# Performance work log

Hardware: AMD Instinct MI355X
Metric: run time of the kernel (lower is better)

Reference implementation:

```python
import jax, jax.numpy as jnp
import numpy as np
from jax import lax

STRIDE = 2  # down_sample_stride
MATMUL_NORM = True


def maxpool2d_5d(x, s):
    # x: [B, T, C, H, W]; kernel=s, stride=s, padding=(s-1)//2 == 0 for s=2
    return lax.reduce_window(
        x, -jnp.inf, lax.max,
        window_dimensions=(1, 1, 1, s, s),
        window_strides=(1, 1, 1, s, s),
        padding='VALID')


def setup_inputs() -> dict:
    key = jax.random.key(0)
    k1, k2, k3, k4 = jax.random.split(key, 4)
    B, T, Ck, Cv, H, W = 2, 4, 64, 256, 64, 64
    return {
        'memory_keys': jax.random.normal(k1, (B, T, Ck, H, W), jnp.float32),
        'memory_values': jax.random.normal(k2, (B, T, Cv, H, W), jnp.float32),
        'query_key': jax.random.normal(k3, (B, Ck, H, W), jnp.float32),
        'query_value': jax.random.normal(k4, (B, Cv, H, W), jnp.float32),
    }


def reference(memory_keys, memory_values, query_key, query_value):
    B, T, Ck, oH, oW = memory_keys.shape
    Cv = memory_values.shape[2]
    # down-sample memory bank (max pool, stride 2, no padding)
    mk = maxpool2d_5d(memory_keys, STRIDE)   # [B,T,Ck,h,w]
    mv = maxpool2d_5d(memory_values, STRIDE) # [B,T,Cv,h,w]
    h, w = mk.shape[-2], mk.shape[-1]
    M = T * h * w
    N = oH * oH  # code uses ori_height*ori_height (square assumed)
    # permute(0,2,1,3,4).view(B,Ck,M).permute(0,2,1) -> [B, M, Ck]
    mk = mk.transpose(0, 2, 1, 3, 4).reshape(B, Ck, M).transpose(0, 2, 1)
    qk = query_key.reshape(B, Ck, N)
    attn = jnp.einsum('bmc,bcn->bmn', mk, qk)  # [B, M, N]
    if MATMUL_NORM:
        attn = attn * (Ck ** -0.5)
    attn = jax.nn.softmax(attn, axis=1)  # softmax over memory positions
    mv = mv.transpose(0, 2, 1, 3, 4).reshape(B, Cv, M)
    memory = jnp.einsum('bcm,bmn->bcn', mv, attn).reshape(B, Cv, oH, oW)
    return jnp.concatenate([query_value, memory], axis=1)  # [B, 2*Cv, H, W]
```

## Files before the change

### kernel.cpp

```cpp
#include <hip/hip_runtime.h>
#include <hip/hip_bf16.h>

typedef unsigned short u16;
typedef unsigned int   u32;
typedef __attribute__((ext_vector_type(8))) short  bf16x8;
typedef __attribute__((ext_vector_type(4))) float  floatx4;

#define NB 2
#define NT 4
#define CK 64
#define CV 256
#define HH 64
#define WW 64
#define MM 4096
#define NN 4096
#define SCALE 0.125f
#define SHIFT 4.0f
#define OUT_B 2097152
#define NW 64
#define NIT 32

__device__ __forceinline__ u16 f2b(float f) {
    __hip_bfloat16 h = __float2bfloat16(f);
    union { __hip_bfloat16 h; u16 u; } v; v.h = h; return v.u;
}

#define PRE_K 65536
#define PRE_V 589824
#define PRE_T 1114112

__global__ void prep(const float* __restrict__ mk, const float* __restrict__ mv,
                     const float4* __restrict__ qv,
                     u16* __restrict__ pk2, u16* __restrict__ vt,
                     float* __restrict__ out) {
    int u = blockIdx.x * 256 + threadIdx.x;
    if (u < PRE_K) {
        int m = u & 4095, cb8 = (u >> 12) & 7, b = u >> 15;
        int t = m >> 10, hh = (m >> 5) & 31, ww = m & 31;
        const float* s0 = mk + ((size_t)((b*NT + t)*CK + cb8*8))*(HH*WW)
                             + (2*hh)*WW + 2*ww;
        bf16x8 fr;
        #pragma unroll
        for (int i = 0; i < 8; ++i) {
            const float* s = s0 + (size_t)i*(HH*WW);
            float2 r0 = *(const float2*)s;
            float2 r1 = *(const float2*)(s + WW);
            fr[i] = (short)f2b(fmaxf(fmaxf(r0.x, r0.y), fmaxf(r1.x, r1.y)));
        }
        *(bf16x8*)(pk2 + ((size_t)(b*8 + cb8)*MM + m)*8) = fr;
    } else if (u < PRE_V) {
        int u2 = u - PRE_K;
        int m4 = u2 & 1023, c = (u2 >> 10) & 255, b = u2 >> 18;
        int t = m4 >> 8, hh = (m4 >> 3) & 31, w8 = m4 & 7;
        const float* s0 = mv + ((size_t)((b*NT + t)*CV + c))*(HH*WW)
                             + (2*hh)*WW + 8*w8;
        float4 a0 = *(const float4*)(s0);
        float4 a1 = *(const float4*)(s0 + 4);
        float4 b0 = *(const float4*)(s0 + WW);
        float4 b1 = *(const float4*)(s0 + WW + 4);
        ushort4 r;
        r.x = f2b(fmaxf(fmaxf(a0.x, a0.y), fmaxf(b0.x, b0.y)));
        r.y = f2b(fmaxf(fmaxf(a0.z, a0.w), fmaxf(b0.z, b0.w)));
        r.z = f2b(fmaxf(fmaxf(a1.x, a1.y), fmaxf(b1.x, b1.y)));
        r.w = f2b(fmaxf(fmaxf(a1.z, a1.w), fmaxf(b1.z, b1.w)));
        *(ushort4*)(vt + ((size_t)(b*CV + c)*MM) + m4*4) = r;
    } else {
        int u3 = u - PRE_V;
        int b = u3 >> 18, ru = u3 & 262143;
        ((float4*)out)[(size_t)b*(OUT_B/4) + ru] = qv[u3];
    }
}

__device__ __forceinline__ void qk_phase(bf16x8 k0, bf16x8 k1,
        const bf16x8 (&qf)[2][4], float (&sacc)[4],
        u16* __restrict__ Pd, int lrow, int cbw, int sw)
{
    #pragma unroll
    for (int t = 0; t < 4; ++t) {
        floatx4 s = __builtin_amdgcn_mfma_f32_16x16x32_bf16(
                        k0, qf[0][t], (floatx4){0.f,0.f,0.f,0.f}, 0, 0, 0);
        s = __builtin_amdgcn_mfma_f32_16x16x32_bf16(k1, qf[1][t], s, 0, 0, 0);
        float p0 = __expf(s[0]*SCALE - SHIFT);
        float p1 = __expf(s[1]*SCALE - SHIFT);
        float p2 = __expf(s[2]*SCALE - SHIFT);
        float p3 = __expf(s[3]*SCALE - SHIFT);
        sacc[t] += (p0 + p1) + (p2 + p3);
        u32 d0 = (u32)f2b(p0) | ((u32)f2b(p1) << 16);
        u32 d1 = (u32)f2b(p2) | ((u32)f2b(p3) << 16);
        *(uint2*)&Pd[(t*16 + lrow)*128 + ((cbw ^ sw) << 2)] = make_uint2(d0, d1);
    }
}

__device__ __forceinline__ void pv_phase(const bf16x8 (&vf)[4],
        floatx4 (&oacc)[4], const u16* __restrict__ Ps,
        int lrow, int quad, int sw)
{
    #pragma unroll
    for (int cc = 0; cc < 4; ++cc) {
        bf16x8 pf[4];
        #pragma unroll
        for (int t = 0; t < 4; ++t) {
            int cb = (cc << 3) + (quad << 1);
            pf[t] = *(const bf16x8*)&Ps[(t*16 + lrow)*128 + ((cb ^ sw) << 2)];
        }
        __builtin_amdgcn_s_setprio(1);
        #pragma unroll
        for (int t = 0; t < 4; ++t)
            oacc[t] = __builtin_amdgcn_mfma_f32_16x16x32_bf16(
                          vf[cc], pf[t], oacc[t], 0, 0, 0);
        __builtin_amdgcn_s_setprio(0);
    }
}

__launch_bounds__(512, 2)
__global__ void attn_v3(const u16* __restrict__ pk2, const u16* __restrict__ vt,
                        const float* __restrict__ qk, float* __restrict__ out) {
    const int bid = blockIdx.x;
    const int xcd = bid & 7, grp = bid >> 3;
    const int b   = xcd >> 2, cs = (xcd >> 1) & 1;
    const int ntile = (xcd & 1) * 32 + grp;
    const int tid = threadIdx.x, w = tid >> 6, l = tid & 63;
    const int lrow = l & 15, quad = l >> 4;
    const int n0 = ntile * NW;
    const int sw  = lrow << 1;
    const int cbw = (w << 2) + quad;

    __shared__ u16  P[2][NW * 128];
    __shared__ float sums_s[8][NW];

    bf16x8 qf[2][4];
    const float* qb = qk + (size_t)b * CK * NN + n0;
    #pragma unroll
    for (int cc = 0; cc < 2; ++cc)
        #pragma unroll
        for (int t = 0; t < 4; ++t)
            #pragma unroll
            for (int i = 0; i < 8; ++i) {
                int c = cc*32 + quad*8 + i;
                qf[cc][t][i] = (short)f2b(qb[(size_t)c*NN + t*16 + lrow]);
            }

    const u16* pkb  = pk2 + (size_t)b * (8*MM*8);
    const int  mrw  = w*16 + lrow;
    const u16* vrow = vt + ((size_t)b*CV + cs*128 + w*16 + lrow)*MM + quad*8;

    floatx4 oacc[4];
    #pragma unroll
    for (int t = 0; t < 4; ++t) oacc[t] = (floatx4){0.f, 0.f, 0.f, 0.f};
    float sacc[4] = {0.f, 0.f, 0.f, 0.f};

    bf16x8 k0 = *(const bf16x8*)(pkb + ((size_t)quad*MM + mrw)*8);
    bf16x8 k1 = *(const bf16x8*)(pkb + ((size_t)(quad+4)*MM + mrw)*8);
    bf16x8 vf[4];
    #pragma unroll
    for (int cc = 0; cc < 4; ++cc)
        vf[cc] = *(const bf16x8*)(vrow + cc*32);
    qk_phase(k0, k1, qf, sacc, P[0], lrow, cbw, sw);

    for (int it = 0; it < NIT - 1; ++it) {
        __syncthreads();
        const int mb2 = (it + 1) << 7;
        bf16x8 k0n = *(const bf16x8*)(pkb + ((size_t)quad*MM + mb2 + mrw)*8);
        bf16x8 k1n = *(const bf16x8*)(pkb + ((size_t)(quad+4)*MM + mb2 + mrw)*8);
        bf16x8 vn[4];
        #pragma unroll
        for (int cc = 0; cc < 4; ++cc)
            vn[cc] = *(const bf16x8*)(vrow + mb2 + cc*32);
        pv_phase(vf, oacc, P[it & 1], lrow, quad, sw);
        qk_phase(k0n, k1n, qf, sacc, P[(it + 1) & 1], lrow, cbw, sw);
        #pragma unroll
        for (int cc = 0; cc < 4; ++cc) vf[cc] = vn[cc];
    }
    __syncthreads();
    pv_phase(vf, oacc, P[(NIT - 1) & 1], lrow, quad, sw);

    #pragma unroll
    for (int t = 0; t < 4; ++t) {
        float v = sacc[t];
        v += __shfl_xor(v, 16, 64);
        v += __shfl_xor(v, 32, 64);
        if (l < 16) sums_s[w][t*16 + l] = v;
    }
    __syncthreads();
    float inv[4];
    #pragma unroll
    for (int t = 0; t < 4; ++t) {
        float d = 0.f;
        #pragma unroll
        for (int w2 = 0; w2 < 8; ++w2) d += sums_s[w2][t*16 + lrow];
        inv[t] = 1.0f / d;
    }

    float* ob = out + ((size_t)(b*512 + 256 + cs*128))*NN + n0;
    #pragma unroll
    for (int t = 0; t < 4; ++t)
        #pragma unroll
        for (int r = 0; r < 4; ++r) {
            int c_loc = w*16 + quad*4 + r;
            ob[(size_t)c_loc*NN + t*16 + lrow] = oacc[t][r] * inv[t];
        }
}


__global__ void pool_v_f32(const float* __restrict__ src, float* __restrict__ out) {
    int e = blockIdx.x * 256 + threadIdx.x;
    int c = e & 255;
    int r = e >> 8;
    int ww = r & 31;  int hh = (r >> 5) & 31;
    int t  = (r >> 10) & 3;  int b = r >> 12;
    int m  = r & (MM - 1);
    const float* s = src + ((size_t)(((b*NT + t)*CV + c)*HH + 2*hh))*WW + 2*ww;
    out[(size_t)b*OUT_B + (size_t)m*CV + c] = fmaxf(fmaxf(s[0], s[1]), fmaxf(s[WW], s[WW+1]));
}

__global__ void pool_k_f32(const float* __restrict__ src, float* __restrict__ dst) {
    int e = blockIdx.x * 256 + threadIdx.x;
    int c = e & 63;
    int r = e >> 6;
    int ww = r & 31;  int hh = (r >> 5) & 31;
    int t  = (r >> 10) & 3;  int b = r >> 12;
    const float* s = src + ((size_t)(((b*NT + t)*CK + c)*HH + 2*hh))*WW + 2*ww;
    dst[e] = fmaxf(fmaxf(s[0], s[1]), fmaxf(s[WW], s[WW+1]));
}

__global__ void copy_qv_f32(const float4* __restrict__ src, float4* __restrict__ dst) {
    int u = blockIdx.x * 256 + threadIdx.x;
    int b  = u >> 18;
    int ru = u & 262143;
    dst[(size_t)b * (OUT_B/4) + ru] = src[u];
}

template<bool STAGED_K>
__launch_bounds__(256)
__global__ void attn_old(const float* __restrict__ pk,
                         const float* __restrict__ mk,
                         const float* __restrict__ qk,
                         float* __restrict__ out) {
    __shared__ __align__(16) float q_lds[CK][4];
    __shared__ __align__(16) float sarr[4][MM];
    __shared__ float inv_l[4];

    const int tid = threadIdx.x;
    const int blk = blockIdx.x;
    const int b   = blk >> 10;
    const int n0  = (blk & 1023) << 2;

    {
        int c = tid >> 2, qi = tid & 3;
        q_lds[c][qi] = qk[((size_t)(b*CK + c))*NN + n0 + qi];
    }
    __syncthreads();

    #pragma unroll
    for (int i = 0; i < 16; ++i) {
        int m = tid + (i << 8);
        float a0 = 0.f, a1 = 0.f, a2 = 0.f, a3 = 0.f;
        if (STAGED_K) {
            const float4* k4 = reinterpret_cast<const float4*>(pk + ((size_t)b*MM + m)*CK);
            #pragma unroll
            for (int cc = 0; cc < 16; ++cc) {
                float4 kv = k4[cc];
                int c = cc*4;
                float4 q0 = *reinterpret_cast<const float4*>(&q_lds[c][0]);
                float4 q1 = *reinterpret_cast<const float4*>(&q_lds[c+1][0]);
                float4 q2 = *reinterpret_cast<const float4*>(&q_lds[c+2][0]);
                float4 q3 = *reinterpret_cast<const float4*>(&q_lds[c+3][0]);
                a0 += kv.x*q0.x + kv.y*q1.x + kv.z*q2.x + kv.w*q3.x;
                a1 += kv.x*q0.y + kv.y*q1.y + kv.z*q2.y + kv.w*q3.y;
                a2 += kv.x*q0.z + kv.y*q1.z + kv.z*q2.z + kv.w*q3.z;
                a3 += kv.x*q0.w + kv.y*q1.w + kv.z*q2.w + kv.w*q3.w;
            }
        } else {
            int ww = m & 31, hh = (m >> 5) & 31, t = m >> 10;
            const float* base = mk + ((size_t)((b*NT + t)*CK)*HH + 2*hh)*WW + 2*ww;
            for (int c = 0; c < CK; ++c) {
                const float* s = base + (size_t)c*HH*WW;
                float kv = fmaxf(fmaxf(s[0], s[1]), fmaxf(s[WW], s[WW+1]));
                float4 q = *reinterpret_cast<const float4*>(&q_lds[c][0]);
                a0 += kv*q.x; a1 += kv*q.y; a2 += kv*q.z; a3 += kv*q.w;
            }
        }
        sarr[0][m] = a0*SCALE;
        sarr[1][m] = a1*SCALE;
        sarr[2][m] = a2*SCALE;
        sarr[3][m] = a3*SCALE;
    }
    __syncthreads();

    const int wave = tid >> 6, lane = tid & 63;
    float mx = -3.0e38f;
    for (int m = lane; m < MM; m += 64) mx = fmaxf(mx, sarr[wave][m]);
    #pragma unroll
    for (int off = 32; off > 0; off >>= 1) mx = fmaxf(mx, __shfl_xor(mx, off, 64));
    float ls = 0.f;
    for (int m = lane; m < MM; m += 64) {
        float p = __expf(sarr[wave][m] - mx);
        sarr[wave][m] = p;
        ls += p;
    }
    #pragma unroll
    for (int off = 32; off > 0; off >>= 1) ls += __shfl_xor(ls, off, 64);
    if (lane == 0) inv_l[wave] = 1.0f / ls;
    __syncthreads();

    const int c4 = lane;
    const float4* vb = reinterpret_cast<const float4*>(out + (size_t)b*OUT_B) + c4;
    const float* prow = sarr[wave];
    float a0 = 0.f, a1 = 0.f, a2 = 0.f, a3 = 0.f;
    for (int m = 0; m < MM; m += 4) {
        float4 p4 = *reinterpret_cast<const float4*>(prow + m);
        const float4* vp = vb + (size_t)m*(CV/4);
        float4 v0 = vp[0], v1 = vp[CV/4], v2 = vp[CV/2], v3 = vp[3*(CV/4)];
        a0 += p4.x*v0.x + p4.y*v1.x + p4.z*v2.x + p4.w*v3.x;
        a1 += p4.x*v0.y + p4.y*v1.y + p4.z*v2.y + p4.w*v3.y;
        a2 += p4.x*v0.z + p4.y*v1.z + p4.z*v2.z + p4.w*v3.z;
        a3 += p4.x*v0.w + p4.y*v1.w + p4.z*v2.w + p4.w*v3.w;
    }

    float inv = inv_l[wave];
    int n = n0 + wave;
    size_t ob = ((size_t)(b*512 + 256 + c4*4))*NN + n;
    out[ob]        = a0*inv;
    out[ob + NN]   = a1*inv;
    out[ob + 2*NN] = a2*inv;
    out[ob + 3*NN] = a3*inv;
}


extern "C" void kernel_launch(void* const* d_in, const int* in_sizes, int n_in,
                              void* d_out, int out_size, void* d_ws, size_t ws_size,
                              hipStream_t stream) {
    const float* mk = (const float*)d_in[0];
    const float* mv = (const float*)d_in[1];
    const float* qk = (const float*)d_in[2];
    const float* qv = (const float*)d_in[3];
    float* out = (float*)d_out;

    u16* pk2 = (u16*)d_ws;
    u16* vt  = pk2 + (size_t)NB*8*MM*8;
    const size_t need = ((size_t)NB*8*MM*8 + (size_t)NB*CV*MM) * sizeof(u16);

    if (ws_size >= need) {
        prep<<<PRE_T/256, 256, 0, stream>>>(mk, mv, (const float4*)qv, pk2, vt, out);
        attn_v3<<<256, 512, 0, stream>>>(pk2, vt, qk, out);
    } else {
        const size_t pk_bytes = (size_t)NB*MM*CK*sizeof(float);
        const bool staged = (ws_size >= pk_bytes);
        float* pk = (float*)d_ws;
        pool_v_f32<<<(NB*MM*CV)/256, 256, 0, stream>>>(mv, out);
        if (staged) {
            pool_k_f32<<<(NB*MM*CK)/256, 256, 0, stream>>>(mk, pk);
            attn_old<true ><<<NB*(NN/4), 256, 0, stream>>>(pk, mk, qk, out);
        } else {
            attn_old<false><<<NB*(NN/4), 256, 0, stream>>>(pk, mk, qk, out);
        }
        copy_qv_f32<<<((NB*CV*HH*WW)/4)/256, 256, 0, stream>>>((const float4*)qv, (float4*)out);
    }
}
```

Before: 143.7 us.

## Split attention over memory dimension into two halves with partial-sum epilogue

The attention kernel now splits the M (memory position) loop into two halves, launching 512 blocks instead of 256, each writing unnormalized partial outputs and row sums to workspace. A new epilogue kernel combines the two halves and normalizes into the output. Launch bounds are raised to target 4 blocks per CU, and exp is computed via exp2f with a fused scale and shift constant. This targets under-occupancy of the GPU (256 blocks on a large device), at the cost of an extra kernel launch and a round trip of 16 MB of partials through memory.

```diff
diff --git a/kernel.cpp b/kernel.cpp
--- a/kernel.cpp
+++ b/kernel.cpp
@@ -1,5 +1,6 @@
 #include <hip/hip_runtime.h>
 #include <hip/hip_bf16.h>
+#include <math.h>
 
 typedef unsigned short u16;
 typedef unsigned int   u32;
@@ -18,7 +19,9 @@
 #define SHIFT 4.0f
 #define OUT_B 2097152
 #define NW 64
-#define NIT 32
+#define ITG 16
+#define C1 0.18033688011112042f
+#define C2 (-5.770780163555853f)
 
 __device__ __forceinline__ u16 f2b(float f) {
     __hip_bfloat16 h = __float2bfloat16(f);
@@ -80,10 +83,10 @@
         floatx4 s = __builtin_amdgcn_mfma_f32_16x16x32_bf16(
                         k0, qf[0][t], (floatx4){0.f,0.f,0.f,0.f}, 0, 0, 0);
         s = __builtin_amdgcn_mfma_f32_16x16x32_bf16(k1, qf[1][t], s, 0, 0, 0);
-        float p0 = __expf(s[0]*SCALE - SHIFT);
-        float p1 = __expf(s[1]*SCALE - SHIFT);
-        float p2 = __expf(s[2]*SCALE - SHIFT);
-        float p3 = __expf(s[3]*SCALE - SHIFT);
+        float p0 = exp2f(__builtin_fmaf(s[0], C1, C2));
+        float p1 = exp2f(__builtin_fmaf(s[1], C1, C2));
+        float p2 = exp2f(__builtin_fmaf(s[2], C1, C2));
+        float p3 = exp2f(__builtin_fmaf(s[3], C1, C2));
         sacc[t] += (p0 + p1) + (p2 + p3);
         u32 d0 = (u32)f2b(p0) | ((u32)f2b(p1) << 16);
         u32 d1 = (u32)f2b(p2) | ((u32)f2b(p3) << 16);
@@ -112,20 +115,24 @@
     }
 }
 
-__launch_bounds__(512, 2)
-__global__ void attn_v3(const u16* __restrict__ pk2, const u16* __restrict__ vt,
-                        const float* __restrict__ qk, float* __restrict__ out) {
+__launch_bounds__(512, 4)
+__global__ void attn_v8(const u16* __restrict__ pk2, const u16* __restrict__ vt,
+                        const float* __restrict__ qk,
+                        float* __restrict__ part, float* __restrict__ sums) {
     const int bid = blockIdx.x;
-    const int xcd = bid & 7, grp = bid >> 3;
-    const int b   = xcd >> 2, cs = (xcd >> 1) & 1;
-    const int ntile = (xcd & 1) * 32 + grp;
+    const int xcd = bid & 7;
+    const int b  = (xcd >> 2) & 1;
+    const int cs = (xcd >> 1) & 1;
+    const int ms = xcd & 1;
+    const int ntile = bid >> 3;
     const int tid = threadIdx.x, w = tid >> 6, l = tid & 63;
     const int lrow = l & 15, quad = l >> 4;
     const int n0 = ntile * NW;
     const int sw  = lrow << 1;
     const int cbw = (w << 2) + quad;
-
-    __shared__ u16  P[2][NW * 128];
+    const int mstart = ms << 11;
+
+    __shared__ __align__(16) u16 P[2][NW * 128];
     __shared__ float sums_s[8][NW];
 
     bf16x8 qf[2][4];
@@ -141,8 +148,9 @@
             }
 
     const u16* pkb  = pk2 + (size_t)b * (8*MM*8);
-    const int  mrw  = w*16 + lrow;
-    const u16* vrow = vt + ((size_t)b*CV + cs*128 + w*16 + lrow)*MM + quad*8;
+    const int  mrw  = mstart + w*16 + lrow;
+    const u16* vrow = vt + ((size_t)b*CV + cs*128 + w*16 + lrow)*MM
+                         + mstart + quad*8;
 
     floatx4 oacc[4];
     #pragma unroll
@@ -157,7 +165,7 @@
         vf[cc] = *(const bf16x8*)(vrow + cc*32);
     qk_phase(k0, k1, qf, sacc, P[0], lrow, cbw, sw);
 
-    for (int it = 0; it < NIT - 1; ++it) {
+    for (int it = 0; it < ITG - 1; ++it) {
         __syncthreads();
         const int mb2 = (it + 1) << 7;
         bf16x8 k0n = *(const bf16x8*)(pkb + ((size_t)quad*MM + mb2 + mrw)*8);
@@ -172,7 +180,7 @@
         for (int cc = 0; cc < 4; ++cc) vf[cc] = vn[cc];
     }
     __syncthreads();
-    pv_phase(vf, oacc, P[(NIT - 1) & 1], lrow, quad, sw);
+    pv_phase(vf, oacc, P[(ITG - 1) & 1], lrow, quad, sw);
 
     #pragma unroll
     for (int t = 0; t < 4; ++t) {
@@ -182,23 +190,46 @@
         if (l < 16) sums_s[w][t*16 + l] = v;
     }
     __syncthreads();
-    float inv[4];
-    #pragma unroll
-    for (int t = 0; t < 4; ++t) {
-        float d = 0.f;
-        #pragma unroll
-        for (int w2 = 0; w2 < 8; ++w2) d += sums_s[w2][t*16 + lrow];
-        inv[t] = 1.0f / d;
-    }
-
-    float* ob = out + ((size_t)(b*512 + 256 + cs*128))*NN + n0;
+
+    float* pb = part + ((size_t)((((ms*NB + b)*2 + cs)*64) + ntile)) * (128*64);
     #pragma unroll
     for (int t = 0; t < 4; ++t)
         #pragma unroll
         for (int r = 0; r < 4; ++r) {
             int c_loc = w*16 + quad*4 + r;
-            ob[(size_t)c_loc*NN + t*16 + lrow] = oacc[t][r] * inv[t];
-        }
+            pb[c_loc*64 + t*16 + lrow] = oacc[t][r];
+        }
+    if (cs == 0 && tid < 64) {
+        float sv = 0.f;
+        #pragma unroll
+        for (int w2 = 0; w2 < 8; ++w2) sv += sums_s[w2][tid];
+        sums[((size_t)((ms*NB + b)*64 + ntile))*64 + tid] = sv;
+    }
+}
+
+__global__ void epilogue2(const float* __restrict__ part,
+                          const float* __restrict__ sums,
+                          float* __restrict__ out) {
+    int e = blockIdx.x * 256 + threadIdx.x;
+    int nl4 = e & 15;
+    int nt  = (e >> 4) & 63;
+    int c   = (e >> 10) & 255;
+    int b   = e >> 18;
+    int cs = c >> 7, cl = c & 127;
+    const float4* p4 = (const float4*)part;
+    const float4* s4 = (const float4*)sums;
+    size_t t0 = (size_t)(((0*NB + b)*2 + cs)*64 + nt);
+    size_t t1 = (size_t)(((1*NB + b)*2 + cs)*64 + nt);
+    float4 u0 = p4[t0*2048 + cl*16 + nl4];
+    float4 u1 = p4[t1*2048 + cl*16 + nl4];
+    float4 d0 = s4[((size_t)((0*NB + b)*64 + nt))*16 + nl4];
+    float4 d1 = s4[((size_t)((1*NB + b)*64 + nt))*16 + nl4];
+    float4 r;
+    r.x = (u0.x + u1.x) / (d0.x + d1.x);
+    r.y = (u0.y + u1.y) / (d0.y + d1.y);
+    r.z = (u0.z + u1.z) / (d0.z + d1.z);
+    r.w = (u0.w + u1.w) / (d0.w + d1.w);
+    ((float4*)out)[(size_t)(b*512 + 256 + c)*1024 + nt*16 + nl4] = r;
 }
 
 
@@ -338,11 +369,15 @@
 
     u16* pk2 = (u16*)d_ws;
     u16* vt  = pk2 + (size_t)NB*8*MM*8;
-    const size_t need = ((size_t)NB*8*MM*8 + (size_t)NB*CV*MM) * sizeof(u16);
+    float* part = (float*)(vt + (size_t)NB*CV*MM);
+    float* sums = part + 4194304;
+    const size_t need = ((size_t)NB*8*MM*8 + (size_t)NB*CV*MM) * sizeof(u16)
+                      + (4194304 + 16384) * sizeof(float);
 
     if (ws_size >= need) {
         prep<<<PRE_T/256, 256, 0, stream>>>(mk, mv, (const float4*)qv, pk2, vt, out);
-        attn_v3<<<256, 512, 0, stream>>>(pk2, vt, qk, out);
+        attn_v8<<<512, 512, 0, stream>>>(pk2, vt, qk, part, sums);
+        epilogue2<<<524288/256, 256, 0, stream>>>(part, sums, out);
     } else {
         const size_t pk_bytes = (size_t)NB*MM*CK*sizeof(float);
         const bool staged = (ws_size >= pk_bytes);
```

Measured after the change: 143.4 us. Within noise of the previous version (-0.2%).
